# Kernel optimization log

Hardware: AMD Instinct MI355X
Metric: run time of the kernel (lower is better)

Reference implementation:

```python
import jax, jax.numpy as jnp
import numpy as np

B, S, D_MODEL = 2, 1024, 512
HEAD = 8
DEPTH = D_MODEL // HEAD  # 64
NFEAT = 64


def _make_orf(rng, n_features, depth):
    # Mirrors OrthogonalRandomFeature: QR of uniform blocks, scaled by norms of gaussian rows.
    n, rem = divmod(n_features, depth)
    blocks = []
    for _ in range(n):
        q, _ = np.linalg.qr(rng.random((depth, depth)))
        blocks.append(q)
    if rem > 0:
        q, _ = np.linalg.qr(rng.random((depth, depth)))
        blocks.append(q[:rem])
    orf = np.concatenate(blocks, axis=0)
    mult = np.linalg.norm(rng.standard_normal((n_features, depth)), axis=1)
    return jnp.asarray(mult[:, None] * orf, dtype=jnp.float32)


def setup_inputs() -> dict:
    key = jax.random.key(0)
    ks = jax.random.split(key, 12)
    rng = np.random.default_rng(0)
    scale = 0.02
    inp = {
        "query": jax.random.normal(ks[0], (B, S, D_MODEL), dtype=jnp.float32),
        "key": jax.random.normal(ks[1], (B, S, D_MODEL), dtype=jnp.float32),
        "value": jax.random.normal(ks[2], (B, S, D_MODEL), dtype=jnp.float32),
        "Wq": jax.random.normal(ks[3], (DEPTH, DEPTH), dtype=jnp.float32) * scale,
        "bq": jnp.zeros((DEPTH,), dtype=jnp.float32),
        "Wk": jax.random.normal(ks[4], (DEPTH, DEPTH), dtype=jnp.float32) * scale,
        "bk": jnp.zeros((DEPTH,), dtype=jnp.float32),
        "Wv": jax.random.normal(ks[5], (DEPTH, DEPTH), dtype=jnp.float32) * scale,
        "bv": jnp.zeros((DEPTH,), dtype=jnp.float32),
        "orf_q": _make_orf(rng, NFEAT, DEPTH),
        "orf_k": _make_orf(rng, NFEAT, DEPTH),
        "Wfc": jax.random.normal(ks[6], (D_MODEL, D_MODEL), dtype=jnp.float32) * scale,
        "bfc": jnp.zeros((D_MODEL,), dtype=jnp.float32),
        "causal": 1,
    }
    return inp


def _kernel_fn(x, orf):
    # x: [n,h,s,d], orf: [f,d]; normalization uses ORF.shape[-1] = depth
    norm = 1.0 / (orf.shape[-1] ** 0.25)
    out = jnp.einsum('nhsd,fd->nhsf', x * norm, orf)
    return jax.nn.relu(out) + 0.001


def _causal_attention(q, k, v):
    # q,k: [n,h,s,f]; v: [n,h,s,d]
    k_cumsum = jnp.cumsum(k, axis=-2)                    # [n,h,s,f]
    x = jnp.einsum('nhkf,nhkd->nhkfd', k, v)             # [n,h,s,f,d]
    x = jnp.cumsum(x, axis=-3)
    x = x / k_cumsum[..., None]
    return jnp.einsum('nhqfd,nhqf->nhqd', x, q)          # [n,h,s,d]


def _bidirectional_attention(q, k, v):
    kt_i = jnp.sum(k, axis=-2)                           # [n,h,f]
    norm = 1.0 / jnp.einsum('nhqf,nhf->nhq', q, kt_i)    # [n,h,s]
    k_v = jnp.einsum('nhkf,nhkd->nhfd', k, v)            # [n,h,f,d]
    return jnp.einsum('nhfd,nhqf,nhq->nhqd', k_v, q, norm)


def reference(query, key, value, Wq, bq, Wk, bk, Wv, bv, orf_q, orf_k, Wfc, bfc, causal):
    b, s, _ = query.shape
    depth = Wq.shape[0]
    head = query.shape[-1] // depth
    # [b,s,d_model] -> [b,h,s,depth]
    q = query.reshape(b, s, head, depth).transpose(0, 2, 1, 3)
    k = key.reshape(b, s, head, depth).transpose(0, 2, 1, 3)
    v = value.reshape(b, s, head, depth).transpose(0, 2, 1, 3)
    # per-head Linear on depth (torch: x @ W.T + b)
    q = jnp.einsum('nhsd,ed->nhse', q, Wq) + bq
    k = jnp.einsum('nhsd,ed->nhse', k, Wk) + bk
    v = jnp.einsum('nhsd,ed->nhse', v, Wv) + bv
    q = _kernel_fn(q, orf_q)
    k = _kernel_fn(k, orf_k)
    if causal:
        out = _causal_attention(q, k, v)
    else:
        out = _bidirectional_attention(q, k, v)
    out = out.transpose(0, 2, 1, 3).reshape(b, s, head * depth)
    return jnp.einsum('nse,oe->nso', out, Wfc) + bfc
```

## Files before the change

### kernel.cpp

```cpp
#include <hip/hip_runtime.h>


#define BB 2
#define SS 1024
#define HH 8
#define DD 64
#define FF 64
#define DM 512
#define NCH 16

typedef __bf16 bf16_t;
typedef __attribute__((ext_vector_type(8))) __bf16 bf16x8;
typedef __attribute__((ext_vector_type(4))) __bf16 bf16x4;
typedef __attribute__((ext_vector_type(4))) float f32x4;

#define MFMA16(a,b,c) __builtin_amdgcn_mfma_f32_16x16x32_bf16((a),(b),(c),0,0,0)

__device__ inline bf16x8 cvt_f32x8(const float* p){
    const float4* p4 = (const float4*)p;
    float4 x = p4[0], y = p4[1];
    bf16x8 r;
    r[0]=(__bf16)x.x; r[1]=(__bf16)x.y; r[2]=(__bf16)x.z; r[3]=(__bf16)x.w;
    r[4]=(__bf16)y.x; r[5]=(__bf16)y.y; r[6]=(__bf16)y.z; r[7]=(__bf16)y.w;
    return r;
}

__global__ __launch_bounds__(256) void kfuse(
    const float* __restrict__ orf_q, const float* __restrict__ orf_k,
    const float* __restrict__ Wq, const float* __restrict__ bq,
    const float* __restrict__ Wk, const float* __restrict__ bk,
    const float* __restrict__ Wv, const float* __restrict__ Wfc,
    bf16_t* __restrict__ Mtq, bf16_t* __restrict__ Mtk,
    float* __restrict__ cq, float* __restrict__ ck,
    bf16_t* __restrict__ WvB, bf16_t* __restrict__ WfcB)
{
    const int tid = threadIdx.x, bid = blockIdx.x;
    if (bid < 2) {
        const float* ORF = bid ? orf_k : orf_q;
        const float* W   = bid ? Wk : Wq;
        const float* bb  = bid ? bk : bq;
        bf16_t* Mt = bid ? Mtk : Mtq;
        float* cc  = bid ? ck : cq;
        const float norm = 0.35355339059327373f;
        const int f = tid >> 2, d0 = (tid & 3) * 16;
        float acc[16];
        #pragma unroll
        for (int j=0;j<16;j++) acc[j]=0.f;
        float bacc = 0.f;
        for (int e=0;e<64;e++){
            float oe = ORF[f*64+e];
            const float* wr = W + e*64 + d0;
            #pragma unroll
            for (int j=0;j<16;j++) acc[j] += oe*wr[j];
            bacc += oe*bb[e];
        }
        #pragma unroll
        for (int j=0;j<16;j++) Mt[f*64+d0+j] = (__bf16)(norm*acc[j]);
        if ((tid&3)==0) cc[f] = norm*bacc;
    } else if (bid == 2) {
        for (int i=tid;i<4096;i+=256) WvB[i] = (__bf16)Wv[i];
    } else {
        const float4* W4 = (const float4*)Wfc;
        for (int i=(bid-3)*256+tid; i<65536; i+=13*256){
            float4 v = W4[i];
            bf16x4 o; o[0]=(__bf16)v.x; o[1]=(__bf16)v.y; o[2]=(__bf16)v.z; o[3]=(__bf16)v.w;
            *(bf16x4*)(WfcB + 4*i) = o;
        }
    }
}

__global__ __launch_bounds__(256) void kproj(
    const float* __restrict__ q_in, const float* __restrict__ k_in,
    const float* __restrict__ v_in,
    const bf16_t* __restrict__ Mtq, const float* __restrict__ cq,
    const bf16_t* __restrict__ Mtk, const float* __restrict__ ck,
    const bf16_t* __restrict__ WvB, const float* __restrict__ bv,
    bf16_t* __restrict__ PHI_Q, bf16_t* __restrict__ PHI_K,
    bf16_t* __restrict__ PHI_KT, bf16_t* __restrict__ VPT)
{
    __shared__ bf16_t kt[64*72];
    const int tid = threadIdx.x;
    const int l = tid & 63;
    const int w = __builtin_amdgcn_readfirstlane(tid >> 6);
    const int qd = l >> 4, m = l & 15;
    const int bid = blockIdx.x;
    const int bh = bid >> 4, stile = bid & 15;
    const int b = bh >> 3, h = bh & 7;
    const int s0 = stile*64;
    const int sw = s0 + w*16;

    {
        const float* xp = q_in + ((size_t)(b*SS + sw + m))*DM + h*DD;
        bf16x8 a0 = cvt_f32x8(xp + qd*8);
        bf16x8 a1 = cvt_f32x8(xp + 32 + qd*8);
        #pragma unroll
        for (int nt=0;nt<4;nt++){
            const int f = nt*16 + m;
            float cb = cq[f];
            f32x4 acc = {cb,cb,cb,cb};
            acc = MFMA16(a0, *(const bf16x8*)(Mtq + f*64 + qd*8), acc);
            acc = MFMA16(a1, *(const bf16x8*)(Mtq + f*64 + 32 + qd*8), acc);
            #pragma unroll
            for (int r=0;r<4;r++){
                float v = acc[r];
                v = (v>0.f)?v:0.f; v += 0.001f;
                PHI_Q[((size_t)bh*SS + sw + qd*4 + r)*FF + f] = (__bf16)v;
            }
        }
    }
    {
        const float* xp = k_in + ((size_t)(b*SS + sw + m))*DM + h*DD;
        bf16x8 a0 = cvt_f32x8(xp + qd*8);
        bf16x8 a1 = cvt_f32x8(xp + 32 + qd*8);
        #pragma unroll
        for (int nt=0;nt<4;nt++){
            const int f = nt*16 + m;
            float cb = ck[f];
            f32x4 acc = {cb,cb,cb,cb};
            acc = MFMA16(a0, *(const bf16x8*)(Mtk + f*64 + qd*8), acc);
            acc = MFMA16(a1, *(const bf16x8*)(Mtk + f*64 + 32 + qd*8), acc);
            #pragma unroll
            for (int r=0;r<4;r++){
                float v = acc[r];
                v = (v>0.f)?v:0.f; v += 0.001f;
                __bf16 h16 = (__bf16)v;
                PHI_K[((size_t)bh*SS + sw + qd*4 + r)*FF + f] = h16;
                kt[f*72 + w*16 + qd*4 + r] = h16;
            }
        }
    }
    __syncthreads();
    {
        const int f = tid >> 2, sg = tid & 3;
        bf16x8 v0 = *(bf16x8*)&kt[f*72 + sg*16];
        bf16x8 v1 = *(bf16x8*)&kt[f*72 + sg*16 + 8];
        bf16_t* dst = PHI_KT + ((size_t)bh*64 + f)*SS + s0 + sg*16;
        *(bf16x8*)dst = v0; *(bf16x8*)(dst+8) = v1;
    }
    __syncthreads();
    {
        const float* xp = v_in + ((size_t)(b*SS + sw + m))*DM + h*DD;
        bf16x8 a0 = cvt_f32x8(xp + qd*8);
        bf16x8 a1 = cvt_f32x8(xp + 32 + qd*8);
        #pragma unroll
        for (int nt=0;nt<4;nt++){
            const int e = nt*16 + m;
            float cb = bv[e];
            f32x4 acc = {cb,cb,cb,cb};
            acc = MFMA16(a0, *(const bf16x8*)(WvB + e*64 + qd*8), acc);
            acc = MFMA16(a1, *(const bf16x8*)(WvB + e*64 + 32 + qd*8), acc);
            #pragma unroll
            for (int r=0;r<4;r++)
                kt[e*72 + w*16 + qd*4 + r] = (__bf16)acc[r];
        }
    }
    __syncthreads();
    {
        const int d = tid >> 2, sg = tid & 3;
        bf16x8 v0 = *(bf16x8*)&kt[d*72 + sg*16];
        bf16x8 v1 = *(bf16x8*)&kt[d*72 + sg*16 + 8];
        bf16_t* dst = VPT + ((size_t)bh*64 + d)*SS + s0 + sg*16;
        *(bf16x8*)dst = v0; *(bf16x8*)(dst+8) = v1;
    }
}

__global__ __launch_bounds__(256) void kchunksum(
    const bf16_t* __restrict__ PHI_KT, const bf16_t* __restrict__ VPT,
    float* __restrict__ CST, float* __restrict__ KCS)
{
    __shared__ float dsT[64*68];
    __shared__ float part[256];
    const int tid = threadIdx.x;
    const int l = tid & 63;
    const int w = __builtin_amdgcn_readfirstlane(tid >> 6);
    const int qd = l >> 4, m = l & 15;
    const int bid = blockIdx.x;
    const int bh = bid >> 4, ch = bid & 15;
    const int cs0 = ch*64;

    const bf16_t* ka = PHI_KT + ((size_t)bh*64 + w*16 + m)*SS + cs0;
    bf16x8 a0 = *(const bf16x8*)(ka + qd*8);
    bf16x8 a1 = *(const bf16x8*)(ka + 32 + qd*8);
    #pragma unroll
    for (int nt=0;nt<4;nt++){
        const bf16_t* vb = VPT + ((size_t)bh*64 + nt*16 + m)*SS + cs0;
        f32x4 acc = {0.f,0.f,0.f,0.f};
        acc = MFMA16(a0, *(const bf16x8*)(vb + qd*8), acc);
        acc = MFMA16(a1, *(const bf16x8*)(vb + 32 + qd*8), acc);
        #pragma unroll
        for (int r=0;r<4;r++)
            dsT[(nt*16+m)*68 + w*16 + qd*4 + r] = acc[r];
    }
    {
        const int f = tid & 63, sg = tid >> 6;
        const bf16_t* kp = PHI_KT + ((size_t)bh*64 + f)*SS + cs0 + sg*16;
        bf16x8 x0 = *(const bf16x8*)kp;
        bf16x8 x1 = *(const bf16x8*)(kp+8);
        float sm = 0.f;
        #pragma unroll
        for (int j=0;j<8;j++) sm += (float)x0[j] + (float)x1[j];
        part[sg*64 + f] = sm;
    }
    __syncthreads();
    if (tid < 64)
        KCS[(size_t)bid*64 + tid] = part[tid] + part[64+tid] + part[128+tid] + part[192+tid];
    {
        const int d = tid >> 2, F = (tid & 3) * 16;
        float* dst = CST + ((size_t)bid*64 + d)*64 + F;
        #pragma unroll
        for (int j=0;j<4;j++)
            *(float4*)(dst + 4*j) = *(float4*)&dsT[d*68 + F + 4*j];
    }
}

__global__ __launch_bounds__(256) void kprefix(float* __restrict__ CST, float* __restrict__ KCS)
{
    const int tid = threadIdx.x, bid = blockIdx.x;
    const int bh = bid >> 2, q = bid & 3;
    float4 run = make_float4(0.f, 0.f, 0.f, 0.f);
    const int e4 = q*256 + tid;
    for (int c = 0; c < NCH; c++) {
        float4* p = (float4*)(CST + ((size_t)(bh*NCH + c))*4096) + e4;
        float4 t = *p; *p = run;
        run.x += t.x; run.y += t.y; run.z += t.z; run.w += t.w;
    }
    if (q == 0 && tid < 64) {
        float r = 0.f;
        for (int c = 0; c < NCH; c++) {
            size_t off = ((size_t)(bh*NCH + c))*64 + tid;
            float t = KCS[off]; KCS[off] = r; r += t;
        }
    }
}

__global__ __launch_bounds__(256) void kattn(
    const bf16_t* __restrict__ PHI_Q, const bf16_t* __restrict__ PHI_K,
    const bf16_t* __restrict__ PHI_KT, const bf16_t* __restrict__ VPT,
    const float* __restrict__ CST, const float* __restrict__ KCS,
    bf16_t* __restrict__ O)
{
    __shared__ float kct[64*67];
    __shared__ bf16_t qnl[64*72];
    __shared__ bf16_t sA[64*72];
    __shared__ float part[256];
    const int tid = threadIdx.x;
    const int l = tid & 63;
    const int w = __builtin_amdgcn_readfirstlane(tid >> 6);
    const int qd = l >> 4, m = l & 15;
    const int bid = blockIdx.x;
    const int bh = bid >> 4, ch = bid & 15;
    const int cs0 = ch*64;

    {
        const int f = tid >> 2, sg = tid & 3;
        const bf16_t* kp = PHI_KT + ((size_t)bh*64 + f)*SS + cs0 + sg*16;
        bf16x8 x0 = *(const bf16x8*)kp;
        bf16x8 x1 = *(const bf16x8*)(kp+8);
        #pragma unroll
        for (int j=0;j<8;j++){
            kct[f*67 + sg*16 + j]     = (float)x0[j];
            kct[f*67 + sg*16 + 8 + j] = (float)x1[j];
        }
    }
    __syncthreads();
    {
        const int f = tid >> 2, sg = tid & 3;
        float v[16];
        #pragma unroll
        for (int j=0;j<16;j++) v[j] = kct[f*67 + sg*16 + j];
        #pragma unroll
        for (int j=1;j<16;j++) v[j] += v[j-1];
        part[f*4 + sg] = v[15];
        __syncthreads();
        float offs = KCS[(size_t)bid*64 + f];
        if (sg > 0) offs += part[f*4 + 0];
        if (sg > 1) offs += part[f*4 + 1];
        if (sg > 2) offs += part[f*4 + 2];
        #pragma unroll
        for (int j=0;j<16;j++) kct[f*67 + sg*16 + j] = offs + v[j];
    }
    __syncthreads();
    {
        const int sr = tid >> 2, F = (tid & 3) * 16;
        const bf16_t* qp = PHI_Q + ((size_t)bh*SS + cs0 + sr)*FF + F;
        bf16x8 x0 = *(const bf16x8*)qp;
        bf16x8 x1 = *(const bf16x8*)(qp+8);
        bf16x8 o0, o1;
        #pragma unroll
        for (int j=0;j<8;j++){
            o0[j] = (__bf16)((float)x0[j] / kct[(F+j)*67 + sr]);
            o1[j] = (__bf16)((float)x1[j] / kct[(F+8+j)*67 + sr]);
        }
        *(bf16x8*)&qnl[sr*72 + F]     = o0;
        *(bf16x8*)&qnl[sr*72 + F + 8] = o1;
    }
    __syncthreads();

    bf16x8 qa0 = *(bf16x8*)&qnl[(w*16+m)*72 + qd*8];
    bf16x8 qa1 = *(bf16x8*)&qnl[(w*16+m)*72 + 32 + qd*8];

    #pragma unroll
    for (int nt=0;nt<4;nt++){
        const bf16_t* kb = PHI_K + ((size_t)bh*SS + cs0 + nt*16 + m)*FF;
        f32x4 acc = {0.f,0.f,0.f,0.f};
        acc = MFMA16(qa0, *(const bf16x8*)(kb + qd*8), acc);
        acc = MFMA16(qa1, *(const bf16x8*)(kb + 32 + qd*8), acc);
        const int t_loc = nt*16 + m;
        #pragma unroll
        for (int r=0;r<4;r++){
            const int s_loc = w*16 + qd*4 + r;
            float v = (t_loc <= s_loc) ? acc[r] : 0.f;
            sA[s_loc*72 + t_loc] = (__bf16)v;
        }
    }
    __syncthreads();

    bf16x8 sa0 = *(bf16x8*)&sA[(w*16+m)*72 + qd*8];
    bf16x8 sa1 = *(bf16x8*)&sA[(w*16+m)*72 + 32 + qd*8];

    #pragma unroll
    for (int nt=0;nt<4;nt++){
        const int d = nt*16 + m;
        const bf16_t* vb = VPT + ((size_t)bh*64 + d)*SS + cs0;
        const float* pp = CST + ((size_t)bid*64 + d)*64;
        f32x4 acc = {0.f,0.f,0.f,0.f};
        acc = MFMA16(sa0, *(const bf16x8*)(vb + qd*8), acc);
        acc = MFMA16(sa1, *(const bf16x8*)(vb + 32 + qd*8), acc);
        acc = MFMA16(qa0, cvt_f32x8(pp + qd*8), acc);
        acc = MFMA16(qa1, cvt_f32x8(pp + 32 + qd*8), acc);
        #pragma unroll
        for (int r=0;r<4;r++)
            O[((size_t)bh*SS + cs0 + w*16 + qd*4 + r)*DD + d] = (__bf16)acc[r];
    }
}

__global__ __launch_bounds__(256) void kfc(
    const bf16_t* __restrict__ O, const bf16_t* __restrict__ WfcB,
    const float* __restrict__ bfc, float* __restrict__ out)
{
    const int tid = threadIdx.x;
    const int l = tid & 63;
    const int w = __builtin_amdgcn_readfirstlane(tid >> 6);
    const int qd = l >> 4, m = l & 15;
    const int bid = blockIdx.x;
    const int rb = bid >> 3, cb = bid & 7;
    const int r0 = rb*64 + w*16;

    f32x4 acc[4];
    #pragma unroll
    for (int nt=0;nt<4;nt++){
        float bb = bfc[cb*64 + nt*16 + m];
        acc[nt][0]=bb; acc[nt][1]=bb; acc[nt][2]=bb; acc[nt][3]=bb;
    }
    const int row = r0 + m;
    const int b = row >> 10, s = row & 1023;
    #pragma unroll 2
    for (int c=0;c<16;c++){
        const int h = c >> 1;
        const int doff = (c & 1)*32 + qd*8;
        bf16x8 a = *(const bf16x8*)(O + ((size_t)((b*HH + h)*SS + s))*DD + doff);
        #pragma unroll
        for (int nt=0;nt<4;nt++){
            bf16x8 bfr = *(const bf16x8*)(WfcB + (size_t)(cb*64 + nt*16 + m)*DM + c*32 + qd*8);
            acc[nt] = MFMA16(a, bfr, acc[nt]);
        }
    }
    #pragma unroll
    for (int nt=0;nt<4;nt++){
        #pragma unroll
        for (int r=0;r<4;r++){
            const int rr = r0 + qd*4 + r;
            out[(size_t)rr*DM + cb*64 + nt*16 + m] = acc[nt][r];
        }
    }
}

extern "C" void kernel_launch(void* const* d_in, const int* in_sizes, int n_in,
                              void* d_out, int out_size, void* d_ws, size_t ws_size,
                              hipStream_t stream) {
    const float* q_in  = (const float*)d_in[0];
    const float* k_in  = (const float*)d_in[1];
    const float* v_in  = (const float*)d_in[2];
    const float* Wq    = (const float*)d_in[3];
    const float* bq    = (const float*)d_in[4];
    const float* Wk    = (const float*)d_in[5];
    const float* bk    = (const float*)d_in[6];
    const float* Wv    = (const float*)d_in[7];
    const float* bv    = (const float*)d_in[8];
    const float* orf_q = (const float*)d_in[9];
    const float* orf_k = (const float*)d_in[10];
    const float* Wfc   = (const float*)d_in[11];
    const float* bfc   = (const float*)d_in[12];

    float* CST   = (float*)d_ws;
    float* KCS   = CST + 1048576;
    bf16_t* PHI_Q  = (bf16_t*)(KCS + 16384);
    bf16_t* PHI_K  = PHI_Q + 1048576;
    bf16_t* PHI_KT = PHI_K + 1048576;
    bf16_t* VPT    = PHI_KT + 1048576;
    bf16_t* O      = VPT + 1048576;
    bf16_t* Mtq    = O + 1048576;
    bf16_t* Mtk    = Mtq + 4096;
    bf16_t* WvB    = Mtk + 4096;
    bf16_t* WfcB   = WvB + 4096;
    float* cq      = (float*)(WfcB + 262144);
    float* ck      = cq + 64;

    kfuse<<<16, 256, 0, stream>>>(orf_q, orf_k, Wq, bq, Wk, bk, Wv, Wfc,
                                  Mtq, Mtk, cq, ck, WvB, WfcB);
    kproj<<<256, 256, 0, stream>>>(q_in, k_in, v_in, Mtq, cq, Mtk, ck, WvB, bv,
                                   PHI_Q, PHI_K, PHI_KT, VPT);
    kchunksum<<<256, 256, 0, stream>>>(PHI_KT, VPT, CST, KCS);
    kprefix<<<64, 256, 0, stream>>>(CST, KCS);
    kattn<<<256, 256, 0, stream>>>(PHI_Q, PHI_K, PHI_KT, VPT, CST, KCS, O);
    kfc<<<256, 256, 0, stream>>>(O, WfcB, bfc, (float*)d_out);
}
```

Baseline: 133.5 us.

## Fuse chunk-sum and prefix into attention kernel; split projection into three tasks

```diff
diff --git a/kernel.cpp b/kernel.cpp
--- a/kernel.cpp
+++ b/kernel.cpp
@@ -84,12 +84,14 @@
     const int w = __builtin_amdgcn_readfirstlane(tid >> 6);
     const int qd = l >> 4, m = l & 15;
     const int bid = blockIdx.x;
-    const int bh = bid >> 4, stile = bid & 15;
+    const int task = bid >> 8;
+    const int rem = bid & 255;
+    const int bh = rem >> 4, stile = rem & 15;
     const int b = bh >> 3, h = bh & 7;
     const int s0 = stile*64;
     const int sw = s0 + w*16;
 
-    {
+    if (task == 0) {
         const float* xp = q_in + ((size_t)(b*SS + sw + m))*DM + h*DD;
         bf16x8 a0 = cvt_f32x8(xp + qd*8);
         bf16x8 a1 = cvt_f32x8(xp + 32 + qd*8);
@@ -107,8 +109,9 @@
                 PHI_Q[((size_t)bh*SS + sw + qd*4 + r)*FF + f] = (__bf16)v;
             }
         }
-    }
-    {
+        return;
+    }
+    if (task == 1) {
         const float* xp = k_in + ((size_t)(b*SS + sw + m))*DM + h*DD;
         bf16x8 a0 = cvt_f32x8(xp + qd*8);
         bf16x8 a1 = cvt_f32x8(xp + 32 + qd*8);
@@ -128,16 +131,14 @@
                 kt[f*72 + w*16 + qd*4 + r] = h16;
             }
         }
-    }
-    __syncthreads();
-    {
+        __syncthreads();
         const int f = tid >> 2, sg = tid & 3;
         bf16x8 v0 = *(bf16x8*)&kt[f*72 + sg*16];
         bf16x8 v1 = *(bf16x8*)&kt[f*72 + sg*16 + 8];
         bf16_t* dst = PHI_KT + ((size_t)bh*64 + f)*SS + s0 + sg*16;
         *(bf16x8*)dst = v0; *(bf16x8*)(dst+8) = v1;
-    }
-    __syncthreads();
+        return;
+    }
     {
         const float* xp = v_in + ((size_t)(b*SS + sw + m))*DM + h*DD;
         bf16x8 a0 = cvt_f32x8(xp + qd*8);
@@ -153,9 +154,7 @@
             for (int r=0;r<4;r++)
                 kt[e*72 + w*16 + qd*4 + r] = (__bf16)acc[r];
         }
-    }
-    __syncthreads();
-    {
+        __syncthreads();
         const int d = tid >> 2, sg = tid & 3;
         bf16x8 v0 = *(bf16x8*)&kt[d*72 + sg*16];
         bf16x8 v1 = *(bf16x8*)&kt[d*72 + sg*16 + 8];
@@ -164,12 +163,17 @@
     }
 }
 
-__global__ __launch_bounds__(256) void kchunksum(
+__global__ __launch_bounds__(256) void kattn(
+    const bf16_t* __restrict__ PHI_Q, const bf16_t* __restrict__ PHI_K,
     const bf16_t* __restrict__ PHI_KT, const bf16_t* __restrict__ VPT,
-    float* __restrict__ CST, float* __restrict__ KCS)
+    bf16_t* __restrict__ O)
 {
-    __shared__ float dsT[64*68];
-    __shared__ float part[256];
+    __shared__ float kct[64*67];
+    __shared__ bf16_t qnl[64*72];
+    __shared__ bf16_t sAl[64*72];
+    __shared__ bf16_t PT[64*72];
+    __shared__ float kcsb[256];
+    __shared__ float scanp[256];
     const int tid = threadIdx.x;
     const int l = tid & 63;
     const int w = __builtin_amdgcn_readfirstlane(tid >> 6);
@@ -178,78 +182,29 @@
     const int bh = bid >> 4, ch = bid & 15;
     const int cs0 = ch*64;
 
-    const bf16_t* ka = PHI_KT + ((size_t)bh*64 + w*16 + m)*SS + cs0;
-    bf16x8 a0 = *(const bf16x8*)(ka + qd*8);
-    bf16x8 a1 = *(const bf16x8*)(ka + 32 + qd*8);
-    #pragma unroll
-    for (int nt=0;nt<4;nt++){
-        const bf16_t* vb = VPT + ((size_t)bh*64 + nt*16 + m)*SS + cs0;
-        f32x4 acc = {0.f,0.f,0.f,0.f};
-        acc = MFMA16(a0, *(const bf16x8*)(vb + qd*8), acc);
-        acc = MFMA16(a1, *(const bf16x8*)(vb + 32 + qd*8), acc);
+    f32x4 pacc[4];
+    #pragma unroll
+    for (int nt=0;nt<4;nt++){ pacc[nt][0]=0.f; pacc[nt][1]=0.f; pacc[nt][2]=0.f; pacc[nt][3]=0.f; }
+    float kpart = 0.f;
+    const bf16_t* kbase = PHI_KT + ((size_t)bh*64 + w*16 + m)*SS;
+    for (int cc = 0; cc < ch; cc++) {
+        bf16x8 a0 = *(const bf16x8*)(kbase + cc*64 + qd*8);
+        bf16x8 a1 = *(const bf16x8*)(kbase + cc*64 + 32 + qd*8);
+        #pragma unroll
+        for (int j=0;j<8;j++) kpart += (float)a0[j] + (float)a1[j];
+        #pragma unroll
+        for (int nt=0;nt<4;nt++){
+            const bf16_t* vb = VPT + ((size_t)bh*64 + nt*16 + m)*SS + cc*64;
+            pacc[nt] = MFMA16(a0, *(const bf16x8*)(vb + qd*8), pacc[nt]);
+            pacc[nt] = MFMA16(a1, *(const bf16x8*)(vb + 32 + qd*8), pacc[nt]);
+        }
+    }
+    kcsb[qd*64 + w*16 + m] = kpart;
+    #pragma unroll
+    for (int nt=0;nt<4;nt++)
         #pragma unroll
         for (int r=0;r<4;r++)
-            dsT[(nt*16+m)*68 + w*16 + qd*4 + r] = acc[r];
-    }
-    {
-        const int f = tid & 63, sg = tid >> 6;
-        const bf16_t* kp = PHI_KT + ((size_t)bh*64 + f)*SS + cs0 + sg*16;
-        bf16x8 x0 = *(const bf16x8*)kp;
-        bf16x8 x1 = *(const bf16x8*)(kp+8);
-        float sm = 0.f;
-        #pragma unroll
-        for (int j=0;j<8;j++) sm += (float)x0[j] + (float)x1[j];
-        part[sg*64 + f] = sm;
-    }
-    __syncthreads();
-    if (tid < 64)
-        KCS[(size_t)bid*64 + tid] = part[tid] + part[64+tid] + part[128+tid] + part[192+tid];
-    {
-        const int d = tid >> 2, F = (tid & 3) * 16;
-        float* dst = CST + ((size_t)bid*64 + d)*64 + F;
-        #pragma unroll
-        for (int j=0;j<4;j++)
-            *(float4*)(dst + 4*j) = *(float4*)&dsT[d*68 + F + 4*j];
-    }
-}
-
-__global__ __launch_bounds__(256) void kprefix(float* __restrict__ CST, float* __restrict__ KCS)
-{
-    const int tid = threadIdx.x, bid = blockIdx.x;
-    const int bh = bid >> 2, q = bid & 3;
-    float4 run = make_float4(0.f, 0.f, 0.f, 0.f);
-    const int e4 = q*256 + tid;
-    for (int c = 0; c < NCH; c++) {
-        float4* p = (float4*)(CST + ((size_t)(bh*NCH + c))*4096) + e4;
-        float4 t = *p; *p = run;
-        run.x += t.x; run.y += t.y; run.z += t.z; run.w += t.w;
-    }
-    if (q == 0 && tid < 64) {
-        float r = 0.f;
-        for (int c = 0; c < NCH; c++) {
-            size_t off = ((size_t)(bh*NCH + c))*64 + tid;
-            float t = KCS[off]; KCS[off] = r; r += t;
-        }
-    }
-}
-
-__global__ __launch_bounds__(256) void kattn(
-    const bf16_t* __restrict__ PHI_Q, const bf16_t* __restrict__ PHI_K,
-    const bf16_t* __restrict__ PHI_KT, const bf16_t* __restrict__ VPT,
-    const float* __restrict__ CST, const float* __restrict__ KCS,
-    bf16_t* __restrict__ O)
-{
-    __shared__ float kct[64*67];
-    __shared__ bf16_t qnl[64*72];
-    __shared__ bf16_t sA[64*72];
-    __shared__ float part[256];
-    const int tid = threadIdx.x;
-    const int l = tid & 63;
-    const int w = __builtin_amdgcn_readfirstlane(tid >> 6);
-    const int qd = l >> 4, m = l & 15;
-    const int bid = blockIdx.x;
-    const int bh = bid >> 4, ch = bid & 15;
-    const int cs0 = ch*64;
+            PT[(nt*16+m)*72 + w*16 + qd*4 + r] = (__bf16)pacc[nt][r];
 
     {
         const int f = tid >> 2, sg = tid & 3;
@@ -263,6 +218,7 @@
         }
     }
     __syncthreads();
+
     {
         const int f = tid >> 2, sg = tid & 3;
         float v[16];
@@ -270,16 +226,17 @@
         for (int j=0;j<16;j++) v[j] = kct[f*67 + sg*16 + j];
         #pragma unroll
         for (int j=1;j<16;j++) v[j] += v[j-1];
-        part[f*4 + sg] = v[15];
+        scanp[f*4 + sg] = v[15];
         __syncthreads();
-        float offs = KCS[(size_t)bid*64 + f];
-        if (sg > 0) offs += part[f*4 + 0];
-        if (sg > 1) offs += part[f*4 + 1];
-        if (sg > 2) offs += part[f*4 + 2];
+        float offs = kcsb[f] + kcsb[64+f] + kcsb[128+f] + kcsb[192+f];
+        if (sg > 0) offs += scanp[f*4 + 0];
+        if (sg > 1) offs += scanp[f*4 + 1];
+        if (sg > 2) offs += scanp[f*4 + 2];
         #pragma unroll
         for (int j=0;j<16;j++) kct[f*67 + sg*16 + j] = offs + v[j];
     }
     __syncthreads();
+
     {
         const int sr = tid >> 2, F = (tid & 3) * 16;
         const bf16_t* qp = PHI_Q + ((size_t)bh*SS + cs0 + sr)*FF + F;
@@ -310,24 +267,23 @@
         for (int r=0;r<4;r++){
             const int s_loc = w*16 + qd*4 + r;
             float v = (t_loc <= s_loc) ? acc[r] : 0.f;
-            sA[s_loc*72 + t_loc] = (__bf16)v;
+            sAl[s_loc*72 + t_loc] = (__bf16)v;
         }
     }
     __syncthreads();
 
-    bf16x8 sa0 = *(bf16x8*)&sA[(w*16+m)*72 + qd*8];
-    bf16x8 sa1 = *(bf16x8*)&sA[(w*16+m)*72 + 32 + qd*8];
+    bf16x8 sa0 = *(bf16x8*)&sAl[(w*16+m)*72 + qd*8];
+    bf16x8 sa1 = *(bf16x8*)&sAl[(w*16+m)*72 + 32 + qd*8];
 
     #pragma unroll
     for (int nt=0;nt<4;nt++){
         const int d = nt*16 + m;
         const bf16_t* vb = VPT + ((size_t)bh*64 + d)*SS + cs0;
-        const float* pp = CST + ((size_t)bid*64 + d)*64;
         f32x4 acc = {0.f,0.f,0.f,0.f};
         acc = MFMA16(sa0, *(const bf16x8*)(vb + qd*8), acc);
         acc = MFMA16(sa1, *(const bf16x8*)(vb + 32 + qd*8), acc);
-        acc = MFMA16(qa0, cvt_f32x8(pp + qd*8), acc);
-        acc = MFMA16(qa1, cvt_f32x8(pp + 32 + qd*8), acc);
+        acc = MFMA16(qa0, *(const bf16x8*)&PT[d*72 + qd*8], acc);
+        acc = MFMA16(qa1, *(const bf16x8*)&PT[d*72 + 32 + qd*8], acc);
         #pragma unroll
         for (int r=0;r<4;r++)
             O[((size_t)bh*SS + cs0 + w*16 + qd*4 + r)*DD + d] = (__bf16)acc[r];
@@ -392,9 +348,7 @@
     const float* Wfc   = (const float*)d_in[11];
     const float* bfc   = (const float*)d_in[12];
 
-    float* CST   = (float*)d_ws;
-    float* KCS   = CST + 1048576;
-    bf16_t* PHI_Q  = (bf16_t*)(KCS + 16384);
+    bf16_t* PHI_Q  = (bf16_t*)d_ws;
     bf16_t* PHI_K  = PHI_Q + 1048576;
     bf16_t* PHI_KT = PHI_K + 1048576;
     bf16_t* VPT    = PHI_KT + 1048576;
@@ -408,10 +362,8 @@
 
     kfuse<<<16, 256, 0, stream>>>(orf_q, orf_k, Wq, bq, Wk, bk, Wv, Wfc,
                                   Mtq, Mtk, cq, ck, WvB, WfcB);
-    kproj<<<256, 256, 0, stream>>>(q_in, k_in, v_in, Mtq, cq, Mtk, ck, WvB, bv,
+    kproj<<<768, 256, 0, stream>>>(q_in, k_in, v_in, Mtq, cq, Mtk, ck, WvB, bv,
                                    PHI_Q, PHI_K, PHI_KT, VPT);
-    kchunksum<<<256, 256, 0, stream>>>(PHI_KT, VPT, CST, KCS);
-    kprefix<<<64, 256, 0, stream>>>(CST, KCS);
-    kattn<<<256, 256, 0, stream>>>(PHI_Q, PHI_K, PHI_KT, VPT, CST, KCS, O);
+    kattn<<<256, 256, 0, stream>>>(PHI_Q, PHI_K, PHI_KT, VPT, O);
     kfc<<<256, 256, 0, stream>>>(O, WfcB, bfc, (float*)d_out);
 }
```

Result: slower. 140.2 us (+5.0%).

## Fuse chunk-sum into projection kernel and use 512-thread blocks for attention and FC

Applied to the files above, without the earlier changes.

```diff
diff --git a/kernel.cpp b/kernel.cpp
--- a/kernel.cpp
+++ b/kernel.cpp
@@ -69,27 +69,32 @@
     }
 }
 
-__global__ __launch_bounds__(256) void kproj(
+__global__ __launch_bounds__(512) void kproj(
     const float* __restrict__ q_in, const float* __restrict__ k_in,
     const float* __restrict__ v_in,
     const bf16_t* __restrict__ Mtq, const float* __restrict__ cq,
     const bf16_t* __restrict__ Mtk, const float* __restrict__ ck,
     const bf16_t* __restrict__ WvB, const float* __restrict__ bv,
     bf16_t* __restrict__ PHI_Q, bf16_t* __restrict__ PHI_K,
-    bf16_t* __restrict__ PHI_KT, bf16_t* __restrict__ VPT)
+    bf16_t* __restrict__ PHI_KT, bf16_t* __restrict__ VPT,
+    float* __restrict__ CST, float* __restrict__ KCS)
 {
     __shared__ bf16_t kt[64*72];
+    __shared__ bf16_t vt[64*72];
+    __shared__ float dsT[64*68];
+    __shared__ float part[256];
     const int tid = threadIdx.x;
     const int l = tid & 63;
     const int w = __builtin_amdgcn_readfirstlane(tid >> 6);
+    const int ww = w & 3;
     const int qd = l >> 4, m = l & 15;
     const int bid = blockIdx.x;
-    const int bh = bid >> 4, stile = bid & 15;
+    const int bh = bid >> 4, ch = bid & 15;
     const int b = bh >> 3, h = bh & 7;
-    const int s0 = stile*64;
-    const int sw = s0 + w*16;
-
-    {
+    const int s0 = ch*64;
+    const int sw = s0 + ww*16;
+
+    if (w < 4) {
         const float* xp = q_in + ((size_t)(b*SS + sw + m))*DM + h*DD;
         bf16x8 a0 = cvt_f32x8(xp + qd*8);
         bf16x8 a1 = cvt_f32x8(xp + 32 + qd*8);
@@ -107,8 +112,7 @@
                 PHI_Q[((size_t)bh*SS + sw + qd*4 + r)*FF + f] = (__bf16)v;
             }
         }
-    }
-    {
+    } else {
         const float* xp = k_in + ((size_t)(b*SS + sw + m))*DM + h*DD;
         bf16x8 a0 = cvt_f32x8(xp + qd*8);
         bf16x8 a1 = cvt_f32x8(xp + 32 + qd*8);
@@ -125,20 +129,19 @@
                 v = (v>0.f)?v:0.f; v += 0.001f;
                 __bf16 h16 = (__bf16)v;
                 PHI_K[((size_t)bh*SS + sw + qd*4 + r)*FF + f] = h16;
-                kt[f*72 + w*16 + qd*4 + r] = h16;
+                kt[f*72 + ww*16 + qd*4 + r] = h16;
             }
         }
     }
     __syncthreads();
-    {
+
+    if (tid < 256) {
         const int f = tid >> 2, sg = tid & 3;
         bf16x8 v0 = *(bf16x8*)&kt[f*72 + sg*16];
         bf16x8 v1 = *(bf16x8*)&kt[f*72 + sg*16 + 8];
         bf16_t* dst = PHI_KT + ((size_t)bh*64 + f)*SS + s0 + sg*16;
         *(bf16x8*)dst = v0; *(bf16x8*)(dst+8) = v1;
-    }
-    __syncthreads();
-    {
+    } else {
         const float* xp = v_in + ((size_t)(b*SS + sw + m))*DM + h*DD;
         bf16x8 a0 = cvt_f32x8(xp + qd*8);
         bf16x8 a1 = cvt_f32x8(xp + 32 + qd*8);
@@ -151,65 +154,53 @@
             acc = MFMA16(a1, *(const bf16x8*)(WvB + e*64 + 32 + qd*8), acc);
             #pragma unroll
             for (int r=0;r<4;r++)
-                kt[e*72 + w*16 + qd*4 + r] = (__bf16)acc[r];
-        }
-    }
-    __syncthreads();
+                vt[e*72 + ww*16 + qd*4 + r] = (__bf16)acc[r];
+        }
+    }
+    __syncthreads();
+
     {
+        const int ft = ww, np = (w >> 2) * 2;
+        bf16x8 a0 = *(bf16x8*)&kt[(ft*16+m)*72 + qd*8];
+        bf16x8 a1 = *(bf16x8*)&kt[(ft*16+m)*72 + 32 + qd*8];
+        #pragma unroll
+        for (int j=0;j<2;j++){
+            const int nt = np + j;
+            f32x4 acc = {0.f,0.f,0.f,0.f};
+            acc = MFMA16(a0, *(bf16x8*)&vt[(nt*16+m)*72 + qd*8], acc);
+            acc = MFMA16(a1, *(bf16x8*)&vt[(nt*16+m)*72 + 32 + qd*8], acc);
+            #pragma unroll
+            for (int r=0;r<4;r++)
+                dsT[(nt*16+m)*68 + ft*16 + qd*4 + r] = acc[r];
+        }
+    }
+    if (tid < 256) {
         const int d = tid >> 2, sg = tid & 3;
-        bf16x8 v0 = *(bf16x8*)&kt[d*72 + sg*16];
-        bf16x8 v1 = *(bf16x8*)&kt[d*72 + sg*16 + 8];
+        bf16x8 v0 = *(bf16x8*)&vt[d*72 + sg*16];
+        bf16x8 v1 = *(bf16x8*)&vt[d*72 + sg*16 + 8];
         bf16_t* dst = VPT + ((size_t)bh*64 + d)*SS + s0 + sg*16;
         *(bf16x8*)dst = v0; *(bf16x8*)(dst+8) = v1;
-    }
-}
-
-__global__ __launch_bounds__(256) void kchunksum(
-    const bf16_t* __restrict__ PHI_KT, const bf16_t* __restrict__ VPT,
-    float* __restrict__ CST, float* __restrict__ KCS)
-{
-    __shared__ float dsT[64*68];
-    __shared__ float part[256];
-    const int tid = threadIdx.x;
-    const int l = tid & 63;
-    const int w = __builtin_amdgcn_readfirstlane(tid >> 6);
-    const int qd = l >> 4, m = l & 15;
-    const int bid = blockIdx.x;
-    const int bh = bid >> 4, ch = bid & 15;
-    const int cs0 = ch*64;
-
-    const bf16_t* ka = PHI_KT + ((size_t)bh*64 + w*16 + m)*SS + cs0;
-    bf16x8 a0 = *(const bf16x8*)(ka + qd*8);
-    bf16x8 a1 = *(const bf16x8*)(ka + 32 + qd*8);
-    #pragma unroll
-    for (int nt=0;nt<4;nt++){
-        const bf16_t* vb = VPT + ((size_t)bh*64 + nt*16 + m)*SS + cs0;
-        f32x4 acc = {0.f,0.f,0.f,0.f};
-        acc = MFMA16(a0, *(const bf16x8*)(vb + qd*8), acc);
-        acc = MFMA16(a1, *(const bf16x8*)(vb + 32 + qd*8), acc);
-        #pragma unroll
-        for (int r=0;r<4;r++)
-            dsT[(nt*16+m)*68 + w*16 + qd*4 + r] = acc[r];
-    }
-    {
-        const int f = tid & 63, sg = tid >> 6;
-        const bf16_t* kp = PHI_KT + ((size_t)bh*64 + f)*SS + cs0 + sg*16;
-        bf16x8 x0 = *(const bf16x8*)kp;
-        bf16x8 x1 = *(const bf16x8*)(kp+8);
+    } else {
+        const int t2 = tid - 256;
+        const int f = t2 & 63, sg = t2 >> 6;
+        bf16x8 x0 = *(bf16x8*)&kt[f*72 + sg*16];
+        bf16x8 x1 = *(bf16x8*)&kt[f*72 + sg*16 + 8];
         float sm = 0.f;
         #pragma unroll
         for (int j=0;j<8;j++) sm += (float)x0[j] + (float)x1[j];
         part[sg*64 + f] = sm;
     }
     __syncthreads();
-    if (tid < 64)
-        KCS[(size_t)bid*64 + tid] = part[tid] + part[64+tid] + part[128+tid] + part[192+tid];
-    {
+
+    if (tid < 256) {
         const int d = tid >> 2, F = (tid & 3) * 16;
         float* dst = CST + ((size_t)bid*64 + d)*64 + F;
         #pragma unroll
         for (int j=0;j<4;j++)
             *(float4*)(dst + 4*j) = *(float4*)&dsT[d*68 + F + 4*j];
+    } else if (tid < 320) {
+        const int f = tid - 256;
+        KCS[(size_t)bid*64 + f] = part[f] + part[64+f] + part[128+f] + part[192+f];
     }
 }
 
@@ -217,23 +208,28 @@
 {
     const int tid = threadIdx.x, bid = blockIdx.x;
     const int bh = bid >> 2, q = bid & 3;
+    const int e4 = q*256 + tid;
+    float4 vals[16];
+    #pragma unroll
+    for (int c = 0; c < NCH; c++)
+        vals[c] = ((float4*)(CST + ((size_t)(bh*NCH + c))*4096))[e4];
     float4 run = make_float4(0.f, 0.f, 0.f, 0.f);
-    const int e4 = q*256 + tid;
+    #pragma unroll
     for (int c = 0; c < NCH; c++) {
-        float4* p = (float4*)(CST + ((size_t)(bh*NCH + c))*4096) + e4;
-        float4 t = *p; *p = run;
-        run.x += t.x; run.y += t.y; run.z += t.z; run.w += t.w;
+        ((float4*)(CST + ((size_t)(bh*NCH + c))*4096))[e4] = run;
+        run.x += vals[c].x; run.y += vals[c].y; run.z += vals[c].z; run.w += vals[c].w;
     }
     if (q == 0 && tid < 64) {
+        float kv[16];
+        #pragma unroll
+        for (int c = 0; c < NCH; c++) kv[c] = KCS[((size_t)(bh*NCH + c))*64 + tid];
         float r = 0.f;
-        for (int c = 0; c < NCH; c++) {
-            size_t off = ((size_t)(bh*NCH + c))*64 + tid;
-            float t = KCS[off]; KCS[off] = r; r += t;
-        }
-    }
-}
-
-__global__ __launch_bounds__(256) void kattn(
+        #pragma unroll
+        for (int c = 0; c < NCH; c++) { KCS[((size_t)(bh*NCH + c))*64 + tid] = r; r += kv[c]; }
+    }
+}
+
+__global__ __launch_bounds__(512) void kattn(
     const bf16_t* __restrict__ PHI_Q, const bf16_t* __restrict__ PHI_K,
     const bf16_t* __restrict__ PHI_KT, const bf16_t* __restrict__ VPT,
     const float* __restrict__ CST, const float* __restrict__ KCS,
@@ -241,17 +237,19 @@
 {
     __shared__ float kct[64*67];
     __shared__ bf16_t qnl[64*72];
-    __shared__ bf16_t sA[64*72];
-    __shared__ float part[256];
+    __shared__ bf16_t sAl[64*72];
+    __shared__ float scanp[256];
     const int tid = threadIdx.x;
     const int l = tid & 63;
     const int w = __builtin_amdgcn_readfirstlane(tid >> 6);
+    const int rt = w & 3;
+    const int np = (w >> 2) * 2;
     const int qd = l >> 4, m = l & 15;
     const int bid = blockIdx.x;
     const int bh = bid >> 4, ch = bid & 15;
     const int cs0 = ch*64;
 
-    {
+    if (tid < 256) {
         const int f = tid >> 2, sg = tid & 3;
         const bf16_t* kp = PHI_KT + ((size_t)bh*64 + f)*SS + cs0 + sg*16;
         bf16x8 x0 = *(const bf16x8*)kp;
@@ -263,24 +261,28 @@
         }
     }
     __syncthreads();
-    {
-        const int f = tid >> 2, sg = tid & 3;
-        float v[16];
-        #pragma unroll
-        for (int j=0;j<16;j++) v[j] = kct[f*67 + sg*16 + j];
-        #pragma unroll
-        for (int j=1;j<16;j++) v[j] += v[j-1];
-        part[f*4 + sg] = v[15];
-        __syncthreads();
-        float offs = KCS[(size_t)bid*64 + f];
-        if (sg > 0) offs += part[f*4 + 0];
-        if (sg > 1) offs += part[f*4 + 1];
-        if (sg > 2) offs += part[f*4 + 2];
-        #pragma unroll
-        for (int j=0;j<16;j++) kct[f*67 + sg*16 + j] = offs + v[j];
-    }
-    __syncthreads();
-    {
+
+    const int f2 = tid >> 2, sg2 = tid & 3;
+    float v16[16];
+    if (tid < 256) {
+        #pragma unroll
+        for (int j=0;j<16;j++) v16[j] = kct[f2*67 + sg2*16 + j];
+        #pragma unroll
+        for (int j=1;j<16;j++) v16[j] += v16[j-1];
+        scanp[f2*4 + sg2] = v16[15];
+    }
+    __syncthreads();
+    if (tid < 256) {
+        float offs = KCS[(size_t)bid*64 + f2];
+        if (sg2 > 0) offs += scanp[f2*4 + 0];
+        if (sg2 > 1) offs += scanp[f2*4 + 1];
+        if (sg2 > 2) offs += scanp[f2*4 + 2];
+        #pragma unroll
+        for (int j=0;j<16;j++) kct[f2*67 + sg2*16 + j] = offs + v16[j];
+    }
+    __syncthreads();
+
+    if (tid < 256) {
         const int sr = tid >> 2, F = (tid & 3) * 16;
         const bf16_t* qp = PHI_Q + ((size_t)bh*SS + cs0 + sr)*FF + F;
         bf16x8 x0 = *(const bf16x8*)qp;
@@ -296,11 +298,12 @@
     }
     __syncthreads();
 
-    bf16x8 qa0 = *(bf16x8*)&qnl[(w*16+m)*72 + qd*8];
-    bf16x8 qa1 = *(bf16x8*)&qnl[(w*16+m)*72 + 32 + qd*8];
-
-    #pragma unroll
-    for (int nt=0;nt<4;nt++){
+    bf16x8 qa0 = *(bf16x8*)&qnl[(rt*16+m)*72 + qd*8];
+    bf16x8 qa1 = *(bf16x8*)&qnl[(rt*16+m)*72 + 32 + qd*8];
+
+    #pragma unroll
+    for (int j=0;j<2;j++){
+        const int nt = np + j;
         const bf16_t* kb = PHI_K + ((size_t)bh*SS + cs0 + nt*16 + m)*FF;
         f32x4 acc = {0.f,0.f,0.f,0.f};
         acc = MFMA16(qa0, *(const bf16x8*)(kb + qd*8), acc);
@@ -308,18 +311,19 @@
         const int t_loc = nt*16 + m;
         #pragma unroll
         for (int r=0;r<4;r++){
-            const int s_loc = w*16 + qd*4 + r;
+            const int s_loc = rt*16 + qd*4 + r;
             float v = (t_loc <= s_loc) ? acc[r] : 0.f;
-            sA[s_loc*72 + t_loc] = (__bf16)v;
-        }
-    }
-    __syncthreads();
-
-    bf16x8 sa0 = *(bf16x8*)&sA[(w*16+m)*72 + qd*8];
-    bf16x8 sa1 = *(bf16x8*)&sA[(w*16+m)*72 + 32 + qd*8];
-
-    #pragma unroll
-    for (int nt=0;nt<4;nt++){
+            sAl[s_loc*72 + t_loc] = (__bf16)v;
+        }
+    }
+    __syncthreads();
+
+    bf16x8 sa0 = *(bf16x8*)&sAl[(rt*16+m)*72 + qd*8];
+    bf16x8 sa1 = *(bf16x8*)&sAl[(rt*16+m)*72 + 32 + qd*8];
+
+    #pragma unroll
+    for (int j=0;j<2;j++){
+        const int nt = np + j;
         const int d = nt*16 + m;
         const bf16_t* vb = VPT + ((size_t)bh*64 + d)*SS + cs0;
         const float* pp = CST + ((size_t)bid*64 + d)*64;
@@ -330,47 +334,48 @@
         acc = MFMA16(qa1, cvt_f32x8(pp + 32 + qd*8), acc);
         #pragma unroll
         for (int r=0;r<4;r++)
-            O[((size_t)bh*SS + cs0 + w*16 + qd*4 + r)*DD + d] = (__bf16)acc[r];
-    }
-}
-
-__global__ __launch_bounds__(256) void kfc(
+            O[((size_t)bh*SS + cs0 + rt*16 + qd*4 + r)*DD + d] = (__bf16)acc[r];
+    }
+}
+
+__global__ __launch_bounds__(512) void kfc(
     const bf16_t* __restrict__ O, const bf16_t* __restrict__ WfcB,
     const float* __restrict__ bfc, float* __restrict__ out)
 {
     const int tid = threadIdx.x;
     const int l = tid & 63;
     const int w = __builtin_amdgcn_readfirstlane(tid >> 6);
+    const int rw = w & 3, cpair = (w >> 2) * 2;
     const int qd = l >> 4, m = l & 15;
     const int bid = blockIdx.x;
     const int rb = bid >> 3, cb = bid & 7;
-    const int r0 = rb*64 + w*16;
-
-    f32x4 acc[4];
-    #pragma unroll
-    for (int nt=0;nt<4;nt++){
-        float bb = bfc[cb*64 + nt*16 + m];
-        acc[nt][0]=bb; acc[nt][1]=bb; acc[nt][2]=bb; acc[nt][3]=bb;
+    const int r0 = rb*64 + rw*16;
+
+    f32x4 acc[2];
+    #pragma unroll
+    for (int j=0;j<2;j++){
+        float bb = bfc[cb*64 + (cpair+j)*16 + m];
+        acc[j][0]=bb; acc[j][1]=bb; acc[j][2]=bb; acc[j][3]=bb;
     }
     const int row = r0 + m;
     const int b = row >> 10, s = row & 1023;
-    #pragma unroll 2
+    #pragma unroll 4
     for (int c=0;c<16;c++){
         const int h = c >> 1;
         const int doff = (c & 1)*32 + qd*8;
         bf16x8 a = *(const bf16x8*)(O + ((size_t)((b*HH + h)*SS + s))*DD + doff);
         #pragma unroll
-        for (int nt=0;nt<4;nt++){
-            bf16x8 bfr = *(const bf16x8*)(WfcB + (size_t)(cb*64 + nt*16 + m)*DM + c*32 + qd*8);
-            acc[nt] = MFMA16(a, bfr, acc[nt]);
-        }
-    }
-    #pragma unroll
-    for (int nt=0;nt<4;nt++){
+        for (int j=0;j<2;j++){
+            bf16x8 bfr = *(const bf16x8*)(WfcB + (size_t)(cb*64 + (cpair+j)*16 + m)*DM + c*32 + qd*8);
+            acc[j] = MFMA16(a, bfr, acc[j]);
+        }
+    }
+    #pragma unroll
+    for (int j=0;j<2;j++){
         #pragma unroll
         for (int r=0;r<4;r++){
             const int rr = r0 + qd*4 + r;
-            out[(size_t)rr*DM + cb*64 + nt*16 + m] = acc[nt][r];
+            out[(size_t)rr*DM + cb*64 + (cpair+j)*16 + m] = acc[j][r];
         }
     }
 }
@@ -394,7 +399,9 @@
 
     float* CST   = (float*)d_ws;
     float* KCS   = CST + 1048576;
-    bf16_t* PHI_Q  = (bf16_t*)(KCS + 16384);
+    float* cq    = KCS + 16384;
+    float* ck    = cq + 64;
+    bf16_t* PHI_Q  = (bf16_t*)(ck + 64);
     bf16_t* PHI_K  = PHI_Q + 1048576;
     bf16_t* PHI_KT = PHI_K + 1048576;
     bf16_t* VPT    = PHI_KT + 1048576;
@@ -403,15 +410,12 @@
     bf16_t* Mtk    = Mtq + 4096;
     bf16_t* WvB    = Mtk + 4096;
     bf16_t* WfcB   = WvB + 4096;
-    float* cq      = (float*)(WfcB + 262144);
-    float* ck      = cq + 64;
 
     kfuse<<<16, 256, 0, stream>>>(orf_q, orf_k, Wq, bq, Wk, bk, Wv, Wfc,
                                   Mtq, Mtk, cq, ck, WvB, WfcB);
-    kproj<<<256, 256, 0, stream>>>(q_in, k_in, v_in, Mtq, cq, Mtk, ck, WvB, bv,
-                                   PHI_Q, PHI_K, PHI_KT, VPT);
-    kchunksum<<<256, 256, 0, stream>>>(PHI_KT, VPT, CST, KCS);
+    kproj<<<256, 512, 0, stream>>>(q_in, k_in, v_in, Mtq, cq, Mtk, ck, WvB, bv,
+                                   PHI_Q, PHI_K, PHI_KT, VPT, CST, KCS);
     kprefix<<<64, 256, 0, stream>>>(CST, KCS);
-    kattn<<<256, 256, 0, stream>>>(PHI_Q, PHI_K, PHI_KT, VPT, CST, KCS, O);
-    kfc<<<256, 256, 0, stream>>>(O, WfcB, bfc, (float*)d_out);
-}
+    kattn<<<256, 512, 0, stream>>>(PHI_Q, PHI_K, PHI_KT, VPT, CST, KCS, O);
+    kfc<<<256, 512, 0, stream>>>(O, WfcB, bfc, (float*)d_out);
+}
```

New measurement: 134.0 us. No clear change (+0.4%).
